# Kernel optimization log

Hardware: AMD Instinct MI355X
Metric: run time of the kernel (lower is better)

The kernel has to match this reference:

```python
import jax, jax.numpy as jnp
import numpy as np

PROCESSING_STEPS = 3


def setup_inputs() -> dict:
    key = jax.random.key(0)
    ks = jax.random.split(key, 6)
    N, D, G = 500000, 128, 4096
    x = jax.random.normal(ks[0], (N, D), dtype=jnp.float32)
    # torch LSTM param layout: [4*hidden, input] and [4*hidden, hidden], gates i,f,g,o
    s = 1.0 / np.sqrt(D)
    W_ih = jax.random.uniform(ks[1], (4 * D, 2 * D), minval=-s, maxval=s, dtype=jnp.float32)
    W_hh = jax.random.uniform(ks[2], (4 * D, D), minval=-s, maxval=s, dtype=jnp.float32)
    b_ih = jax.random.uniform(ks[3], (4 * D,), minval=-s, maxval=s, dtype=jnp.float32)
    b_hh = jax.random.uniform(ks[4], (4 * D,), minval=-s, maxval=s, dtype=jnp.float32)
    index = jnp.sort(jax.random.randint(ks[5], (N,), 0, G, dtype=jnp.int64))
    return {"x": x, "W_ih": W_ih, "W_hh": W_hh, "b_ih": b_ih, "b_hh": b_hh,
            "index": index, "dim_size": G}


def _lstm_cell(inp, h, c, W_ih, W_hh, b_ih, b_hh):
    gates = inp @ W_ih.T + h @ W_hh.T + (b_ih + b_hh)  # [G, 4D]
    i, f, g, o = jnp.split(gates, 4, axis=-1)
    c = jax.nn.sigmoid(f) * c + jax.nn.sigmoid(i) * jnp.tanh(g)
    h = jax.nn.sigmoid(o) * jnp.tanh(c)
    return h, c


def reference(x, W_ih, W_hh, b_ih, b_hh, index, dim_size):
    N, D = x.shape
    h = jnp.zeros((dim_size, D), dtype=x.dtype)
    c = jnp.zeros((dim_size, D), dtype=x.dtype)
    q_star = jnp.zeros((dim_size, 2 * D), dtype=x.dtype)
    for _ in range(PROCESSING_STEPS):
        h, c = _lstm_cell(q_star, h, c, W_ih, W_hh, b_ih, b_hh)
        q = h  # [G, D]
        e = jnp.sum(x * q[index], axis=-1)  # [N]
        # segment softmax (numerically stable)
        m = jax.ops.segment_max(e, index, num_segments=dim_size)
        m = jnp.where(jnp.isfinite(m), m, 0.0)  # guard empty segments
        ex = jnp.exp(e - m[index])
        s = jax.ops.segment_sum(ex, index, num_segments=dim_size)
        a = ex / jnp.maximum(s, 1e-16)[index]  # [N]
        r = jax.ops.segment_sum(a[:, None] * x, index, num_segments=dim_size)  # [G, D]
        q_star = jnp.concatenate([q, r], axis=-1)
    return q_star
```

## Files before the change

kernel.cpp:

```cpp
#include <hip/hip_runtime.h>
#include <hip/hip_fp16.h>
#include <math.h>

#define D 128

__device__ __forceinline__ float sigmoidf_(float x) { return 1.f / (1.f + __expf(-x)); }

__global__ void prep_kernel(const float* __restrict__ W_ih, const float* __restrict__ W_hh,
                            const float* __restrict__ b_ih, const float* __restrict__ b_hh,
                            const int* __restrict__ idx, int N, int G,
                            float* __restrict__ Wc, int* __restrict__ seg_off,
                            float* __restrict__ b_sum, float* __restrict__ h1,
                            float* __restrict__ c1) {
    int b = blockIdx.x, t = threadIdx.x;
    if (b < 256) {
        int i = b * 256 + t;
        int j = i >> 7, k = i & (D - 1);
        Wc[i] = W_ih[(size_t)j * (2 * D) + k] + W_hh[i];
    } else if (b < 273) {
        int g = (b - 256) * 256 + t;
        if (g <= G) {
            int lo = 0, hi = N;
            while (lo < hi) {
                int mid = (lo + hi) >> 1;
                if (idx[mid] < g) lo = mid + 1; else hi = mid;
            }
            seg_off[g] = lo;
        }
    } else {
        for (int i = t; i < 4 * D; i += 256) b_sum[i] = b_ih[i] + b_hh[i];
        if (t < D) {
            float bi = b_ih[t] + b_hh[t];
            float bg = b_ih[2 * D + t] + b_hh[2 * D + t];
            float bo = b_ih[3 * D + t] + b_hh[3 * D + t];
            float c = sigmoidf_(bi) * tanhf(bg);
            c1[t] = c;
            h1[t] = sigmoidf_(bo) * tanhf(c);
        }
    }
}

__global__ __launch_bounds__(256) void x_to_h_kernel(const float* __restrict__ x,
                                                     __half* __restrict__ xh,
                                                     size_t total) {
    size_t i = ((size_t)blockIdx.x * 256 + threadIdx.x) * 8;
    if (i >= total) return;
    float4 a = *(const float4*)&x[i];
    float4 b = *(const float4*)&x[i + 4];
    __half2 h[4];
    h[0] = __floats2half2_rn(a.x, a.y);
    h[1] = __floats2half2_rn(a.z, a.w);
    h[2] = __floats2half2_rn(b.x, b.y);
    h[3] = __floats2half2_rn(b.z, b.w);
    *(float4*)&xh[i] = *(float4*)h;
}

__global__ __launch_bounds__(256) void attn_kernel(
    const __half* __restrict__ xh, const int* __restrict__ seg_off,
    const float* __restrict__ q, int q_stride,
    float* __restrict__ r_out, int r_stride, int G) {
    int g = blockIdx.x;
    if (g >= G) return;
    int tid = threadIdx.x;
    int wave = tid >> 6, lane = tid & 63;
    int qg = lane >> 4;
    int c = lane & 15;

    __shared__ float sm[4], ss[4];
    __shared__ float sacc[4][D];

    int start = seg_off[g], end = seg_off[g + 1];
    int count = end - start;
    int chunk = (count + 3) >> 2;
    int wsr = start + wave * chunk;
    int wer = min(wsr + chunk, end);

    const float4* x4 = (const float4*)xh;
    const float* qrow = q + (size_t)g * q_stride;
    float4 q0 = *(const float4*)&qrow[8 * c];
    float4 q1 = *(const float4*)&qrow[8 * c + 4];

    float m = -INFINITY, s = 0.f;
    float acc[8] = {0.f, 0.f, 0.f, 0.f, 0.f, 0.f, 0.f, 0.f};

    if (wsr < wer) {
        int last = wer - 1;
        for (int base = wsr; base < wer; base += 8) {
            int r0 = min(base + qg, last);
            int r1 = min(base + 4 + qg, last);
            float4 v0 = x4[(size_t)r0 * 16 + c];
            float4 v1 = x4[(size_t)r1 * 16 + c];
            const __half2* h0 = (const __half2*)&v0;
            const __half2* h1 = (const __half2*)&v1;
            float2 a0 = __half22float2(h0[0]), a1 = __half22float2(h0[1]);
            float2 a2 = __half22float2(h0[2]), a3 = __half22float2(h0[3]);
            float2 b0 = __half22float2(h1[0]), b1 = __half22float2(h1[1]);
            float2 b2 = __half22float2(h1[2]), b3 = __half22float2(h1[3]);
            float xf0[8] = {a0.x, a0.y, a1.x, a1.y, a2.x, a2.y, a3.x, a3.y};
            float xf1[8] = {b0.x, b0.y, b1.x, b1.y, b2.x, b2.y, b3.x, b3.y};

            float p0 = xf0[0] * q0.x + xf0[1] * q0.y + xf0[2] * q0.z + xf0[3] * q0.w
                     + xf0[4] * q1.x + xf0[5] * q1.y + xf0[6] * q1.z + xf0[7] * q1.w;
            float p1 = xf1[0] * q0.x + xf1[1] * q0.y + xf1[2] * q0.z + xf1[3] * q0.w
                     + xf1[4] * q1.x + xf1[5] * q1.y + xf1[6] * q1.z + xf1[7] * q1.w;
#pragma unroll
            for (int off = 1; off < 16; off <<= 1) {
                p0 += __shfl_xor(p0, off);
                p1 += __shfl_xor(p1, off);
            }
            float p0a = __shfl_xor(p0, 16), p0b = __shfl_xor(p0, 32), p0c = __shfl_xor(p0a, 32);
            float p1a = __shfl_xor(p1, 16), p1b = __shfl_xor(p1, 32), p1c = __shfl_xor(p1a, 32);
            float s00 = (base + qg       < wer) ? p0  : -INFINITY;
            float s01 = (base + (qg ^ 1) < wer) ? p0a : -INFINITY;
            float s02 = (base + (qg ^ 2) < wer) ? p0b : -INFINITY;
            float s03 = (base + (qg ^ 3) < wer) ? p0c : -INFINITY;
            float s10 = (base + 4 + qg       < wer) ? p1  : -INFINITY;
            float s11 = (base + 4 + (qg ^ 1) < wer) ? p1a : -INFINITY;
            float s12 = (base + 4 + (qg ^ 2) < wer) ? p1b : -INFINITY;
            float s13 = (base + 4 + (qg ^ 3) < wer) ? p1c : -INFINITY;

            float mn = fmaxf(fmaxf(fmaxf(s00, s01), fmaxf(s02, s03)),
                             fmaxf(fmaxf(s10, s11), fmaxf(s12, s13)));
            mn = fmaxf(m, mn);
            float al = __expf(m - mn);
            float w00 = __expf(s00 - mn), w01 = __expf(s01 - mn);
            float w02 = __expf(s02 - mn), w03 = __expf(s03 - mn);
            float w10 = __expf(s10 - mn), w11 = __expf(s11 - mn);
            float w12 = __expf(s12 - mn), w13 = __expf(s13 - mn);
            float sg = (w00 + w01) + (w02 + w03) + ((w10 + w11) + (w12 + w13));
            s = s * al + sg;
#pragma unroll
            for (int j = 0; j < 8; ++j)
                acc[j] = acc[j] * al + w00 * xf0[j] + w10 * xf1[j];
            m = mn;
        }
    }
#pragma unroll
    for (int j = 0; j < 8; ++j) {
        acc[j] += __shfl_xor(acc[j], 16);
        acc[j] += __shfl_xor(acc[j], 32);
    }
    if (lane == 0) { sm[wave] = m; ss[wave] = s; }
    if (qg == 0) {
#pragma unroll
        for (int j = 0; j < 8; ++j) sacc[wave][8 * c + j] = acc[j];
    }
    __syncthreads();

    if (tid < D) {
        float m0 = sm[0], m1 = sm[1], m2 = sm[2], m3 = sm[3];
        float mstar = fmaxf(fmaxf(m0, m1), fmaxf(m2, m3));
        float r = 0.f;
        if (mstar > -INFINITY) {
            float e0 = __expf(m0 - mstar), e1 = __expf(m1 - mstar);
            float e2 = __expf(m2 - mstar), e3 = __expf(m3 - mstar);
            float stot = ss[0] * e0 + ss[1] * e1 + ss[2] * e2 + ss[3] * e3;
            float at = sacc[0][tid] * e0 + sacc[1][tid] * e1
                     + sacc[2][tid] * e2 + sacc[3][tid] * e3;
            r = at / fmaxf(stot, 1e-16f);
        }
        r_out[(size_t)g * r_stride + tid] = r;
    }
}

__global__ __launch_bounds__(256) void gates_gemm_kernel(
    const float* __restrict__ A1, int sA1,
    const float* __restrict__ W1,
    const float* __restrict__ A2,
    const float* __restrict__ W2, int sW2,
    const float* __restrict__ bias,
    float* __restrict__ gates) {
    __shared__ float As[32][72];
    __shared__ float Ws[32][72];
    int t = threadIdx.x;
    int tx = t & 15, ty = t >> 4;
    int g0 = blockIdx.x * 64, j0 = blockIdx.y * 64;
    int lr = t & 63;
    int lk = (t >> 6) * 8;

    float acc[4][4];
#pragma unroll
    for (int i = 0; i < 4; ++i)
#pragma unroll
        for (int j = 0; j < 4; ++j) acc[i][j] = 0.f;

    for (int phase = 0; phase < 2; ++phase) {
        const float* A = phase ? A2 : A1;
        int sA = phase ? D : sA1;
        const float* W = phase ? W2 : W1;
        int sW = phase ? sW2 : D;
        for (int kk = 0; kk < D; kk += 32) {
            float4 a0 = *(const float4*)&A[(size_t)(g0 + lr) * sA + kk + lk];
            float4 a1 = *(const float4*)&A[(size_t)(g0 + lr) * sA + kk + lk + 4];
            float4 w0 = *(const float4*)&W[(size_t)(j0 + lr) * sW + kk + lk];
            float4 w1 = *(const float4*)&W[(size_t)(j0 + lr) * sW + kk + lk + 4];
            __syncthreads();
            As[lk + 0][lr] = a0.x; As[lk + 1][lr] = a0.y; As[lk + 2][lr] = a0.z; As[lk + 3][lr] = a0.w;
            As[lk + 4][lr] = a1.x; As[lk + 5][lr] = a1.y; As[lk + 6][lr] = a1.z; As[lk + 7][lr] = a1.w;
            Ws[lk + 0][lr] = w0.x; Ws[lk + 1][lr] = w0.y; Ws[lk + 2][lr] = w0.z; Ws[lk + 3][lr] = w0.w;
            Ws[lk + 4][lr] = w1.x; Ws[lk + 5][lr] = w1.y; Ws[lk + 6][lr] = w1.z; Ws[lk + 7][lr] = w1.w;
            __syncthreads();
#pragma unroll
            for (int k = 0; k < 32; ++k) {
                float4 av = *(const float4*)&As[k][ty * 4];
                float4 bv = *(const float4*)&Ws[k][tx * 4];
                float aa[4] = {av.x, av.y, av.z, av.w};
                float bb[4] = {bv.x, bv.y, bv.z, bv.w};
#pragma unroll
                for (int i = 0; i < 4; ++i)
#pragma unroll
                    for (int j = 0; j < 4; ++j)
                        acc[i][j] = fmaf(aa[i], bb[j], acc[i][j]);
            }
        }
    }
#pragma unroll
    for (int i = 0; i < 4; ++i) {
        size_t row = (size_t)(g0 + ty * 4 + i);
        int jb = j0 + tx * 4;
        float4 o;
        o.x = acc[i][0] + bias[jb + 0];
        o.y = acc[i][1] + bias[jb + 1];
        o.z = acc[i][2] + bias[jb + 2];
        o.w = acc[i][3] + bias[jb + 3];
        *(float4*)&gates[row * 512 + jb] = o;
    }
}

__global__ void cell_kernel(const float* __restrict__ gates,
                            const float* __restrict__ c_prev, int c_stride,
                            float* __restrict__ c_out,
                            float* __restrict__ h_out, int h_stride,
                            int total) {
    int t = blockIdx.x * blockDim.x + threadIdx.x;
    if (t >= total) return;
    int g = t >> 7, k = t & (D - 1);
    const float* grow = gates + (size_t)g * 512;
    float ig = grow[k];
    float fg = grow[D + k];
    float gg = grow[2 * D + k];
    float og = grow[3 * D + k];
    float cp = c_prev[(size_t)g * c_stride + k];
    float c = sigmoidf_(fg) * cp + sigmoidf_(ig) * tanhf(gg);
    float h = sigmoidf_(og) * tanhf(c);
    c_out[t] = c;
    h_out[(size_t)g * h_stride + k] = h;
}

extern "C" void kernel_launch(void* const* d_in, const int* in_sizes, int n_in,
                              void* d_out, int out_size, void* d_ws, size_t ws_size,
                              hipStream_t stream) {
    const float* x      = (const float*)d_in[0];
    const float* W_ih   = (const float*)d_in[1];
    const float* W_hh   = (const float*)d_in[2];
    const float* b_ih   = (const float*)d_in[3];
    const float* b_hh   = (const float*)d_in[4];
    const int*   index  = (const int*)d_in[5];
    int N = in_sizes[5];
    int G = out_size / (2 * D);
    float* out = (float*)d_out;
    size_t totalx = (size_t)N * D;

    float* ws = (float*)d_ws;
    __half* xh    = (__half*)ws;
    float* Wc     = ws + totalx / 2;
    float* b_sum  = Wc + 4 * D * D;
    float* h1     = b_sum + 4 * D;
    float* c1     = h1 + D;
    float* r1     = c1 + D;
    float* h2     = r1 + (size_t)G * D;
    float* c2     = h2 + (size_t)G * D;
    float* r2     = c2 + (size_t)G * D;
    float* gatesb = r2 + (size_t)G * D;
    int* seg_off  = (int*)(gatesb + (size_t)G * 4 * D);
    float* c3     = r1;

    prep_kernel<<<274, 256, 0, stream>>>(W_ih, W_hh, b_ih, b_hh, index, N, G,
                                         Wc, seg_off, b_sum, h1, c1);
    x_to_h_kernel<<<(int)((totalx / 8 + 255) / 256), 256, 0, stream>>>(x, xh, totalx);

    attn_kernel<<<G, 256, 0, stream>>>(xh, seg_off, h1, 0, r1, D, G);

    gates_gemm_kernel<<<dim3(G / 64, 8), 256, 0, stream>>>(
        h1, 0, Wc, r1, W_ih + D, 2 * D, b_sum, gatesb);
    cell_kernel<<<(G * D + 255) / 256, 256, 0, stream>>>(gatesb, c1, 0, c2, h2, D, G * D);
    attn_kernel<<<G, 256, 0, stream>>>(xh, seg_off, h2, D, r2, D, G);

    gates_gemm_kernel<<<dim3(G / 64, 8), 256, 0, stream>>>(
        h2, D, Wc, r2, W_ih + D, 2 * D, b_sum, gatesb);
    cell_kernel<<<(G * D + 255) / 256, 256, 0, stream>>>(gatesb, c2, D, c3, out, 2 * D, G * D);
    attn_kernel<<<G, 256, 0, stream>>>(xh, seg_off, out, 2 * D, out + D, 2 * D, G);
}
```

Baseline: 493.6 us.

## Fuse all three processing steps into one persistent per-group kernel

Replaces the separate x-conversion, attention, gates GEMM and cell kernels with one fused kernel. Each block owns four groups, one wave per group, and keeps h, c, gates and q_star in shared memory across steps. The first attention pass reads fp32 x with nontemporal loads and writes the fp16 copy itself, so the separate conversion pass is gone. The LSTM gates are computed in-block against a transposed concatenated weight matrix, removing the global gate and state round trips. The cost is one wave per segment instead of four, less parallelism within a segment, and weight reads repeated by every block.

```diff
diff --git a/kernel.cpp b/kernel.cpp
--- a/kernel.cpp
+++ b/kernel.cpp
@@ -4,19 +4,33 @@
 
 #define D 128
 
+typedef float f4v __attribute__((ext_vector_type(4)));
+
 __device__ __forceinline__ float sigmoidf_(float x) { return 1.f / (1.f + __expf(-x)); }
+
+__device__ __forceinline__ float4 pack8_to_half8(const float* xf) {
+    __half2 hh[4];
+    hh[0] = __floats2half2_rn(xf[0], xf[1]);
+    hh[1] = __floats2half2_rn(xf[2], xf[3]);
+    hh[2] = __floats2half2_rn(xf[4], xf[5]);
+    hh[3] = __floats2half2_rn(xf[6], xf[7]);
+    return *(float4*)hh;
+}
 
 __global__ void prep_kernel(const float* __restrict__ W_ih, const float* __restrict__ W_hh,
                             const float* __restrict__ b_ih, const float* __restrict__ b_hh,
                             const int* __restrict__ idx, int N, int G,
-                            float* __restrict__ Wc, int* __restrict__ seg_off,
+                            float* __restrict__ WcatT, int* __restrict__ seg_off,
                             float* __restrict__ b_sum, float* __restrict__ h1,
                             float* __restrict__ c1) {
     int b = blockIdx.x, t = threadIdx.x;
     if (b < 256) {
-        int i = b * 256 + t;
-        int j = i >> 7, k = i & (D - 1);
-        Wc[i] = W_ih[(size_t)j * (2 * D) + k] + W_hh[i];
+        int k = b;
+        for (int j = t; j < 512; j += 256) {
+            float v = W_ih[(size_t)j * 256 + k];
+            if (k < 128) v += W_hh[(size_t)j * 128 + k];
+            WcatT[(size_t)k * 512 + j] = v;
+        }
     } else if (b < 273) {
         int g = (b - 256) * 256 + t;
         if (g <= G) {
@@ -40,52 +54,101 @@
     }
 }
 
-__global__ __launch_bounds__(256) void x_to_h_kernel(const float* __restrict__ x,
-                                                     __half* __restrict__ xh,
-                                                     size_t total) {
-    size_t i = ((size_t)blockIdx.x * 256 + threadIdx.x) * 8;
-    if (i >= total) return;
-    float4 a = *(const float4*)&x[i];
-    float4 b = *(const float4*)&x[i + 4];
-    __half2 h[4];
-    h[0] = __floats2half2_rn(a.x, a.y);
-    h[1] = __floats2half2_rn(a.z, a.w);
-    h[2] = __floats2half2_rn(b.x, b.y);
-    h[3] = __floats2half2_rn(b.z, b.w);
-    *(float4*)&xh[i] = *(float4*)h;
-}
-
-__global__ __launch_bounds__(256) void attn_kernel(
-    const __half* __restrict__ xh, const int* __restrict__ seg_off,
-    const float* __restrict__ q, int q_stride,
-    float* __restrict__ r_out, int r_stride, int G) {
-    int g = blockIdx.x;
-    if (g >= G) return;
-    int tid = threadIdx.x;
-    int wave = tid >> 6, lane = tid & 63;
-    int qg = lane >> 4;
-    int c = lane & 15;
-
-    __shared__ float sm[4], ss[4];
-    __shared__ float sacc[4][D];
-
-    int start = seg_off[g], end = seg_off[g + 1];
-    int count = end - start;
-    int chunk = (count + 3) >> 2;
-    int wsr = start + wave * chunk;
-    int wer = min(wsr + chunk, end);
-
-    const float4* x4 = (const float4*)xh;
-    const float* qrow = q + (size_t)g * q_stride;
+__device__ __forceinline__ void online8(const float (&xf0)[8], const float (&xf1)[8],
+                                        const float4 q0, const float4 q1,
+                                        int base, int wer, int qg,
+                                        float& m, float& s, float (&acc)[8]) {
+    float p0 = xf0[0] * q0.x + xf0[1] * q0.y + xf0[2] * q0.z + xf0[3] * q0.w
+             + xf0[4] * q1.x + xf0[5] * q1.y + xf0[6] * q1.z + xf0[7] * q1.w;
+    float p1 = xf1[0] * q0.x + xf1[1] * q0.y + xf1[2] * q0.z + xf1[3] * q0.w
+             + xf1[4] * q1.x + xf1[5] * q1.y + xf1[6] * q1.z + xf1[7] * q1.w;
+#pragma unroll
+    for (int off = 1; off < 16; off <<= 1) {
+        p0 += __shfl_xor(p0, off);
+        p1 += __shfl_xor(p1, off);
+    }
+    float p0a = __shfl_xor(p0, 16), p0b = __shfl_xor(p0, 32), p0c = __shfl_xor(p0a, 32);
+    float p1a = __shfl_xor(p1, 16), p1b = __shfl_xor(p1, 32), p1c = __shfl_xor(p1a, 32);
+    float s00 = (base + qg       < wer) ? p0  : -INFINITY;
+    float s01 = (base + (qg ^ 1) < wer) ? p0a : -INFINITY;
+    float s02 = (base + (qg ^ 2) < wer) ? p0b : -INFINITY;
+    float s03 = (base + (qg ^ 3) < wer) ? p0c : -INFINITY;
+    float s10 = (base + 4 + qg       < wer) ? p1  : -INFINITY;
+    float s11 = (base + 4 + (qg ^ 1) < wer) ? p1a : -INFINITY;
+    float s12 = (base + 4 + (qg ^ 2) < wer) ? p1b : -INFINITY;
+    float s13 = (base + 4 + (qg ^ 3) < wer) ? p1c : -INFINITY;
+
+    float mn = fmaxf(fmaxf(fmaxf(s00, s01), fmaxf(s02, s03)),
+                     fmaxf(fmaxf(s10, s11), fmaxf(s12, s13)));
+    mn = fmaxf(m, mn);
+    float al = __expf(m - mn);
+    float w00 = __expf(s00 - mn), w01 = __expf(s01 - mn);
+    float w02 = __expf(s02 - mn), w03 = __expf(s03 - mn);
+    float w10 = __expf(s10 - mn), w11 = __expf(s11 - mn);
+    float w12 = __expf(s12 - mn), w13 = __expf(s13 - mn);
+    float sg = (w00 + w01) + (w02 + w03) + ((w10 + w11) + (w12 + w13));
+    s = s * al + sg;
+#pragma unroll
+    for (int j = 0; j < 8; ++j)
+        acc[j] = acc[j] * al + w00 * xf0[j] + w10 * xf1[j];
+    m = mn;
+}
+
+__device__ __forceinline__ void attn_finish(float (&acc)[8], float s, int qg, int c,
+                                            float* rdst, bool wr) {
+#pragma unroll
+    for (int j = 0; j < 8; ++j) {
+        acc[j] += __shfl_xor(acc[j], 16);
+        acc[j] += __shfl_xor(acc[j], 32);
+    }
+    if (wr && qg == 0) {
+        float inv = 1.f / fmaxf(s, 1e-16f);
+        float4 o0; o0.x = acc[0] * inv; o0.y = acc[1] * inv; o0.z = acc[2] * inv; o0.w = acc[3] * inv;
+        float4 o1; o1.x = acc[4] * inv; o1.y = acc[5] * inv; o1.z = acc[6] * inv; o1.w = acc[7] * inv;
+        *(float4*)&rdst[8 * c] = o0;
+        *(float4*)&rdst[8 * c + 4] = o1;
+    }
+}
+
+__device__ __forceinline__ void attn_f32(const float* __restrict__ x, __half* __restrict__ xh,
+                                         int start, int end, int qg, int c,
+                                         const float* qrow, float* rdst, bool wr) {
     float4 q0 = *(const float4*)&qrow[8 * c];
     float4 q1 = *(const float4*)&qrow[8 * c + 4];
-
     float m = -INFINITY, s = 0.f;
     float acc[8] = {0.f, 0.f, 0.f, 0.f, 0.f, 0.f, 0.f, 0.f};
-
-    if (wsr < wer) {
-        int last = wer - 1;
-        for (int base = wsr; base < wer; base += 8) {
+    const f4v* x4 = (const f4v*)x;
+    float4* xh4 = (float4*)xh;
+    if (start < end) {
+        int last = end - 1;
+        for (int base = start; base < end; base += 8) {
+            int r0 = min(base + qg, last);
+            int r1 = min(base + 4 + qg, last);
+            f4v f00 = __builtin_nontemporal_load(&x4[(size_t)r0 * 32 + 2 * c]);
+            f4v f01 = __builtin_nontemporal_load(&x4[(size_t)r0 * 32 + 2 * c + 1]);
+            f4v f10 = __builtin_nontemporal_load(&x4[(size_t)r1 * 32 + 2 * c]);
+            f4v f11 = __builtin_nontemporal_load(&x4[(size_t)r1 * 32 + 2 * c + 1]);
+            float xf0[8] = {f00.x, f00.y, f00.z, f00.w, f01.x, f01.y, f01.z, f01.w};
+            float xf1[8] = {f10.x, f10.y, f10.z, f10.w, f11.x, f11.y, f11.z, f11.w};
+            xh4[(size_t)r0 * 16 + c] = pack8_to_half8(xf0);
+            xh4[(size_t)r1 * 16 + c] = pack8_to_half8(xf1);
+            online8(xf0, xf1, q0, q1, base, end, qg, m, s, acc);
+        }
+    }
+    attn_finish(acc, s, qg, c, rdst, wr);
+}
+
+__device__ __forceinline__ void attn_f16(const __half* __restrict__ xh,
+                                         int start, int end, int qg, int c,
+                                         const float* qrow, float* rdst, bool wr) {
+    float4 q0 = *(const float4*)&qrow[8 * c];
+    float4 q1 = *(const float4*)&qrow[8 * c + 4];
+    float m = -INFINITY, s = 0.f;
+    float acc[8] = {0.f, 0.f, 0.f, 0.f, 0.f, 0.f, 0.f, 0.f};
+    const float4* x4 = (const float4*)xh;
+    if (start < end) {
+        int last = end - 1;
+        for (int base = start; base < end; base += 8) {
             int r0 = min(base + qg, last);
             int r1 = min(base + 4 + qg, last);
             float4 v0 = x4[(size_t)r0 * 16 + c];
@@ -98,153 +161,101 @@
             float2 b2 = __half22float2(h1[2]), b3 = __half22float2(h1[3]);
             float xf0[8] = {a0.x, a0.y, a1.x, a1.y, a2.x, a2.y, a3.x, a3.y};
             float xf1[8] = {b0.x, b0.y, b1.x, b1.y, b2.x, b2.y, b3.x, b3.y};
-
-            float p0 = xf0[0] * q0.x + xf0[1] * q0.y + xf0[2] * q0.z + xf0[3] * q0.w
-                     + xf0[4] * q1.x + xf0[5] * q1.y + xf0[6] * q1.z + xf0[7] * q1.w;
-            float p1 = xf1[0] * q0.x + xf1[1] * q0.y + xf1[2] * q0.z + xf1[3] * q0.w
-                     + xf1[4] * q1.x + xf1[5] * q1.y + xf1[6] * q1.z + xf1[7] * q1.w;
-#pragma unroll
-            for (int off = 1; off < 16; off <<= 1) {
-                p0 += __shfl_xor(p0, off);
-                p1 += __shfl_xor(p1, off);
+            online8(xf0, xf1, q0, q1, base, end, qg, m, s, acc);
+        }
+    }
+    attn_finish(acc, s, qg, c, rdst, wr);
+}
+
+__global__ __launch_bounds__(256, 4) void fused_kernel(
+    const float* __restrict__ x, __half* __restrict__ xh,
+    const int* __restrict__ seg_off, const float* __restrict__ WcatT,
+    const float* __restrict__ b_sum, const float* __restrict__ h1,
+    const float* __restrict__ c1, float* __restrict__ out, int G) {
+
+    __shared__ float qs[4][256];
+    __shared__ float cL[4][128];
+    __shared__ float gl[4][512];
+    __shared__ float bL[512];
+
+    int tid = threadIdx.x;
+    int w = tid >> 6, lane = tid & 63;
+    int qg = lane >> 4, c = lane & 15;
+    int gbase = blockIdx.x * 4;
+    int g = gbase + w;
+    bool valid = g < G;
+    int start = 0, end = 0;
+    if (valid) { start = seg_off[g]; end = seg_off[g + 1]; }
+
+    for (int e = tid; e < 512; e += 256) bL[e] = b_sum[e];
+    if (tid < 128) {
+        float hv = h1[tid], cv = c1[tid];
+#pragma unroll
+        for (int s2 = 0; s2 < 4; ++s2) { qs[s2][tid] = hv; cL[s2][tid] = cv; }
+    }
+    __syncthreads();
+
+    int j0 = w * 128 + 2 * lane;
+    const float* wp = WcatT + j0;
+
+    attn_f32(x, xh, start, end, qg, c, &qs[w][0], &qs[w][128], true);
+    __syncthreads();
+
+#pragma unroll 1
+    for (int step = 0; step < 2; ++step) {
+        float a0[4] = {0.f, 0.f, 0.f, 0.f};
+        float a1[4] = {0.f, 0.f, 0.f, 0.f};
+        for (int k = 0; k < 256; k += 4) {
+            float qv[4][4];
+            *(float4*)qv[0] = *(const float4*)&qs[0][k];
+            *(float4*)qv[1] = *(const float4*)&qs[1][k];
+            *(float4*)qv[2] = *(const float4*)&qs[2][k];
+            *(float4*)qv[3] = *(const float4*)&qs[3][k];
+#pragma unroll
+            for (int dk = 0; dk < 4; ++dk) {
+                float2 wv = *(const float2*)&wp[(size_t)(k + dk) * 512];
+#pragma unroll
+                for (int s2 = 0; s2 < 4; ++s2) {
+                    a0[s2] = fmaf(qv[s2][dk], wv.x, a0[s2]);
+                    a1[s2] = fmaf(qv[s2][dk], wv.y, a1[s2]);
+                }
             }
-            float p0a = __shfl_xor(p0, 16), p0b = __shfl_xor(p0, 32), p0c = __shfl_xor(p0a, 32);
-            float p1a = __shfl_xor(p1, 16), p1b = __shfl_xor(p1, 32), p1c = __shfl_xor(p1a, 32);
-            float s00 = (base + qg       < wer) ? p0  : -INFINITY;
-            float s01 = (base + (qg ^ 1) < wer) ? p0a : -INFINITY;
-            float s02 = (base + (qg ^ 2) < wer) ? p0b : -INFINITY;
-            float s03 = (base + (qg ^ 3) < wer) ? p0c : -INFINITY;
-            float s10 = (base + 4 + qg       < wer) ? p1  : -INFINITY;
-            float s11 = (base + 4 + (qg ^ 1) < wer) ? p1a : -INFINITY;
-            float s12 = (base + 4 + (qg ^ 2) < wer) ? p1b : -INFINITY;
-            float s13 = (base + 4 + (qg ^ 3) < wer) ? p1c : -INFINITY;
-
-            float mn = fmaxf(fmaxf(fmaxf(s00, s01), fmaxf(s02, s03)),
-                             fmaxf(fmaxf(s10, s11), fmaxf(s12, s13)));
-            mn = fmaxf(m, mn);
-            float al = __expf(m - mn);
-            float w00 = __expf(s00 - mn), w01 = __expf(s01 - mn);
-            float w02 = __expf(s02 - mn), w03 = __expf(s03 - mn);
-            float w10 = __expf(s10 - mn), w11 = __expf(s11 - mn);
-            float w12 = __expf(s12 - mn), w13 = __expf(s13 - mn);
-            float sg = (w00 + w01) + (w02 + w03) + ((w10 + w11) + (w12 + w13));
-            s = s * al + sg;
-#pragma unroll
-            for (int j = 0; j < 8; ++j)
-                acc[j] = acc[j] * al + w00 * xf0[j] + w10 * xf1[j];
-            m = mn;
-        }
-    }
-#pragma unroll
-    for (int j = 0; j < 8; ++j) {
-        acc[j] += __shfl_xor(acc[j], 16);
-        acc[j] += __shfl_xor(acc[j], 32);
-    }
-    if (lane == 0) { sm[wave] = m; ss[wave] = s; }
-    if (qg == 0) {
-#pragma unroll
-        for (int j = 0; j < 8; ++j) sacc[wave][8 * c + j] = acc[j];
-    }
-    __syncthreads();
-
-    if (tid < D) {
-        float m0 = sm[0], m1 = sm[1], m2 = sm[2], m3 = sm[3];
-        float mstar = fmaxf(fmaxf(m0, m1), fmaxf(m2, m3));
-        float r = 0.f;
-        if (mstar > -INFINITY) {
-            float e0 = __expf(m0 - mstar), e1 = __expf(m1 - mstar);
-            float e2 = __expf(m2 - mstar), e3 = __expf(m3 - mstar);
-            float stot = ss[0] * e0 + ss[1] * e1 + ss[2] * e2 + ss[3] * e3;
-            float at = sacc[0][tid] * e0 + sacc[1][tid] * e1
-                     + sacc[2][tid] * e2 + sacc[3][tid] * e3;
-            r = at / fmaxf(stot, 1e-16f);
-        }
-        r_out[(size_t)g * r_stride + tid] = r;
-    }
-}
-
-__global__ __launch_bounds__(256) void gates_gemm_kernel(
-    const float* __restrict__ A1, int sA1,
-    const float* __restrict__ W1,
-    const float* __restrict__ A2,
-    const float* __restrict__ W2, int sW2,
-    const float* __restrict__ bias,
-    float* __restrict__ gates) {
-    __shared__ float As[32][72];
-    __shared__ float Ws[32][72];
-    int t = threadIdx.x;
-    int tx = t & 15, ty = t >> 4;
-    int g0 = blockIdx.x * 64, j0 = blockIdx.y * 64;
-    int lr = t & 63;
-    int lk = (t >> 6) * 8;
-
-    float acc[4][4];
-#pragma unroll
-    for (int i = 0; i < 4; ++i)
-#pragma unroll
-        for (int j = 0; j < 4; ++j) acc[i][j] = 0.f;
-
-    for (int phase = 0; phase < 2; ++phase) {
-        const float* A = phase ? A2 : A1;
-        int sA = phase ? D : sA1;
-        const float* W = phase ? W2 : W1;
-        int sW = phase ? sW2 : D;
-        for (int kk = 0; kk < D; kk += 32) {
-            float4 a0 = *(const float4*)&A[(size_t)(g0 + lr) * sA + kk + lk];
-            float4 a1 = *(const float4*)&A[(size_t)(g0 + lr) * sA + kk + lk + 4];
-            float4 w0 = *(const float4*)&W[(size_t)(j0 + lr) * sW + kk + lk];
-            float4 w1 = *(const float4*)&W[(size_t)(j0 + lr) * sW + kk + lk + 4];
-            __syncthreads();
-            As[lk + 0][lr] = a0.x; As[lk + 1][lr] = a0.y; As[lk + 2][lr] = a0.z; As[lk + 3][lr] = a0.w;
-            As[lk + 4][lr] = a1.x; As[lk + 5][lr] = a1.y; As[lk + 6][lr] = a1.z; As[lk + 7][lr] = a1.w;
-            Ws[lk + 0][lr] = w0.x; Ws[lk + 1][lr] = w0.y; Ws[lk + 2][lr] = w0.z; Ws[lk + 3][lr] = w0.w;
-            Ws[lk + 4][lr] = w1.x; Ws[lk + 5][lr] = w1.y; Ws[lk + 6][lr] = w1.z; Ws[lk + 7][lr] = w1.w;
-            __syncthreads();
-#pragma unroll
-            for (int k = 0; k < 32; ++k) {
-                float4 av = *(const float4*)&As[k][ty * 4];
-                float4 bv = *(const float4*)&Ws[k][tx * 4];
-                float aa[4] = {av.x, av.y, av.z, av.w};
-                float bb[4] = {bv.x, bv.y, bv.z, bv.w};
-#pragma unroll
-                for (int i = 0; i < 4; ++i)
-#pragma unroll
-                    for (int j = 0; j < 4; ++j)
-                        acc[i][j] = fmaf(aa[i], bb[j], acc[i][j]);
-            }
-        }
-    }
-#pragma unroll
-    for (int i = 0; i < 4; ++i) {
-        size_t row = (size_t)(g0 + ty * 4 + i);
-        int jb = j0 + tx * 4;
-        float4 o;
-        o.x = acc[i][0] + bias[jb + 0];
-        o.y = acc[i][1] + bias[jb + 1];
-        o.z = acc[i][2] + bias[jb + 2];
-        o.w = acc[i][3] + bias[jb + 3];
-        *(float4*)&gates[row * 512 + jb] = o;
-    }
-}
-
-__global__ void cell_kernel(const float* __restrict__ gates,
-                            const float* __restrict__ c_prev, int c_stride,
-                            float* __restrict__ c_out,
-                            float* __restrict__ h_out, int h_stride,
-                            int total) {
-    int t = blockIdx.x * blockDim.x + threadIdx.x;
-    if (t >= total) return;
-    int g = t >> 7, k = t & (D - 1);
-    const float* grow = gates + (size_t)g * 512;
-    float ig = grow[k];
-    float fg = grow[D + k];
-    float gg = grow[2 * D + k];
-    float og = grow[3 * D + k];
-    float cp = c_prev[(size_t)g * c_stride + k];
-    float c = sigmoidf_(fg) * cp + sigmoidf_(ig) * tanhf(gg);
-    float h = sigmoidf_(og) * tanhf(c);
-    c_out[t] = c;
-    h_out[(size_t)g * h_stride + k] = h;
+        }
+        float bx = bL[j0], by = bL[j0 + 1];
+#pragma unroll
+        for (int s2 = 0; s2 < 4; ++s2) {
+            float2 o; o.x = a0[s2] + bx; o.y = a1[s2] + by;
+            *(float2*)&gl[s2][j0] = o;
+        }
+        __syncthreads();
+
+        bool final_step = (step == 1);
+#pragma unroll
+        for (int r2 = 0; r2 < 2; ++r2) {
+            int e = tid + 256 * r2;
+            int s2 = e >> 7, k = e & 127;
+            float ig = gl[s2][k];
+            float fg = gl[s2][128 + k];
+            float gg = gl[s2][256 + k];
+            float og = gl[s2][384 + k];
+            float cp = cL[s2][k];
+            float cc = sigmoidf_(fg) * cp + sigmoidf_(ig) * tanhf(gg);
+            float hh = sigmoidf_(og) * tanhf(cc);
+            cL[s2][k] = cc;
+            qs[s2][k] = hh;
+            if (final_step && (gbase + s2) < G)
+                out[(size_t)(gbase + s2) * 256 + k] = hh;
+        }
+        __syncthreads();
+
+        if (!final_step) {
+            attn_f16(xh, start, end, qg, c, &qs[w][0], &qs[w][128], true);
+        } else {
+            float* rdst = valid ? (out + (size_t)g * 256 + 128) : (float*)&qs[w][128];
+            attn_f16(xh, start, end, qg, c, &qs[w][0], rdst, valid);
+        }
+        __syncthreads();
+    }
 }
 
 extern "C" void kernel_launch(void* const* d_in, const int* in_sizes, int n_in,
@@ -263,31 +274,15 @@
 
     float* ws = (float*)d_ws;
     __half* xh    = (__half*)ws;
-    float* Wc     = ws + totalx / 2;
-    float* b_sum  = Wc + 4 * D * D;
+    float* WcatT  = ws + totalx / 2;
+    float* b_sum  = WcatT + 256 * 512;
     float* h1     = b_sum + 4 * D;
     float* c1     = h1 + D;
-    float* r1     = c1 + D;
-    float* h2     = r1 + (size_t)G * D;
-    float* c2     = h2 + (size_t)G * D;
-    float* r2     = c2 + (size_t)G * D;
-    float* gatesb = r2 + (size_t)G * D;
-    int* seg_off  = (int*)(gatesb + (size_t)G * 4 * D);
-    float* c3     = r1;
+    int* seg_off  = (int*)(c1 + D);
 
     prep_kernel<<<274, 256, 0, stream>>>(W_ih, W_hh, b_ih, b_hh, index, N, G,
-                                         Wc, seg_off, b_sum, h1, c1);
-    x_to_h_kernel<<<(int)((totalx / 8 + 255) / 256), 256, 0, stream>>>(x, xh, totalx);
-
-    attn_kernel<<<G, 256, 0, stream>>>(xh, seg_off, h1, 0, r1, D, G);
-
-    gates_gemm_kernel<<<dim3(G / 64, 8), 256, 0, stream>>>(
-        h1, 0, Wc, r1, W_ih + D, 2 * D, b_sum, gatesb);
-    cell_kernel<<<(G * D + 255) / 256, 256, 0, stream>>>(gatesb, c1, 0, c2, h2, D, G * D);
-    attn_kernel<<<G, 256, 0, stream>>>(xh, seg_off, h2, D, r2, D, G);
-
-    gates_gemm_kernel<<<dim3(G / 64, 8), 256, 0, stream>>>(
-        h2, D, Wc, r2, W_ih + D, 2 * D, b_sum, gatesb);
-    cell_kernel<<<(G * D + 255) / 256, 256, 0, stream>>>(gatesb, c2, D, c3, out, 2 * D, G * D);
-    attn_kernel<<<G, 256, 0, stream>>>(xh, seg_off, out, 2 * D, out + D, 2 * D, G);
-}
+                                         WcatT, seg_off, b_sum, h1, c1);
+
+    int nb = (G + 3) >> 2;
+    fused_kernel<<<nb, 256, 0, stream>>>(x, xh, seg_off, WcatT, b_sum, h1, c1, out, G);
+}
```

Measured after the change: 467.7 us. -5.2%, faster.
